# Performance work log

Hardware: AMD Instinct MI355X
Metric: run time of the kernel (lower is better)

Reference implementation:

```python
import jax, jax.numpy as jnp
import numpy as np

N_NODES = 100000
N_EDGES = 300000
HID = 256
N0, N1, N2 = 40000, 30000, 30000
D0, D1, D2 = 512, 256, 128


def setup_inputs() -> dict:
    key = jax.random.key(0)
    ks = jax.random.split(key, 14)
    s = 0.05  # init scale
    return {
        "feat0": jax.random.normal(ks[0], (N0, D0), jnp.float32),
        "feat1": jax.random.normal(ks[1], (N1, D1), jnp.float32),
        "feat2": jax.random.normal(ks[2], (N2, D2), jnp.float32),
        # per-type Linear(in_dim, HID) params (torch Linear: y = x @ W.T + b)
        "fc_w0": jax.random.normal(ks[3], (HID, D0), jnp.float32) * s,
        "fc_b0": jnp.zeros((HID,), jnp.float32),
        "fc_w1": jax.random.normal(ks[4], (HID, D1), jnp.float32) * s,
        "fc_b1": jnp.zeros((HID,), jnp.float32),
        "fc_w2": jax.random.normal(ks[5], (HID, D2), jnp.float32) * s,
        "fc_b2": jnp.zeros((HID,), jnp.float32),
        # GraphConv 1: weight=False, bias=True
        "gc1_bias": jnp.zeros((HID,), jnp.float32),
        # GraphConv 2: weight (in,out) + bias (DGL convention: feat @ W)
        "gc2_weight": jax.random.normal(ks[6], (HID, HID), jnp.float32) * s,
        "gc2_bias": jnp.zeros((HID,), jnp.float32),
        "semantic_weight": jax.random.normal(ks[7], (1, 5), jnp.float32),
        "src": jax.random.randint(ks[8], (N_EDGES,), 0, N_NODES, jnp.int64),
        "dst": jax.random.randint(ks[9], (N_EDGES,), 0, N_NODES, jnp.int64),
    }


def reference(feat0, feat1, feat2, fc_w0, fc_b0, fc_w1, fc_b1, fc_w2, fc_b2,
              gc1_bias, gc2_weight, gc2_bias, semantic_weight, src, dst):
    # per-type projection then concat along node dim -> [N_NODES, HID]
    h = jnp.concatenate([
        feat0 @ fc_w0.T + fc_b0,
        feat1 @ fc_w1.T + fc_b1,
        feat2 @ fc_w2.T + fc_b2,
    ], axis=0)

    ones = jnp.ones((src.shape[0],), h.dtype)
    deg_out = jnp.maximum(jax.ops.segment_sum(ones, src, num_segments=N_NODES), 1.0)
    deg_in = jnp.maximum(jax.ops.segment_sum(ones, dst, num_segments=N_NODES), 1.0)
    norm_out = jax.lax.rsqrt(deg_out)[:, None]  # D_out^{-1/2}
    norm_in = jax.lax.rsqrt(deg_in)[:, None]    # D_in^{-1/2}

    def gconv(x, W, b):
        # DGL GraphConv, norm='both': D_in^{-1/2} A D_out^{-1/2} x W + b, relu
        msg = (x * norm_out)[src]                                  # [E, HID]
        agg = jax.ops.segment_sum(msg, dst, num_segments=N_NODES)  # [N, HID]
        agg = agg * norm_in
        if W is not None:
            agg = agg @ W
        return jax.nn.relu(agg + b)

    # dropout is identity in eval mode
    h = gconv(h, None, gc1_bias)        # layer 0: weight=False
    h = gconv(h, gc2_weight, gc2_bias)  # layer 1
    return h, semantic_weight
```

## Files before the change

### kernel.cpp

```cpp
#include <hip/hip_runtime.h>
#include <cstdint>

#define HID 256
static constexpr int    NNODES = 100000;
static constexpr int    NEDGES = 300000;
static constexpr size_t NH     = (size_t)NNODES * HID;
static constexpr int    SCAN_B = 256;
static constexpr int    NSBLK  = (NNODES + SCAN_B - 1) / SCAN_B;

typedef __attribute__((ext_vector_type(8))) short bf16x8;
typedef __attribute__((ext_vector_type(4))) float f32x4;

__device__ __forceinline__ unsigned short f2bf(float x) {
    unsigned int u = __float_as_uint(x);
    u += 0x7fffu + ((u >> 16) & 1u);
    return (unsigned short)(u >> 16);
}
__device__ __forceinline__ unsigned int pack2(float a, float b) {
    return (unsigned int)f2bf(a) | ((unsigned int)f2bf(b) << 16);
}
__device__ __forceinline__ float bflo(unsigned int u) { return __uint_as_float(u << 16); }
__device__ __forceinline__ float bfhi(unsigned int u) { return __uint_as_float(u & 0xffff0000u); }

__global__ void zero_i32_k(int* __restrict__ p, int n) {
    int i = blockIdx.x * blockDim.x + threadIdx.x;
    if (i < n) p[i] = 0;
}

__global__ void count_deg_k(const int* __restrict__ src, const int* __restrict__ dst,
                            int* __restrict__ degout, int* __restrict__ degin) {
    int e = blockIdx.x * blockDim.x + threadIdx.x;
    if (e < NEDGES) {
        atomicAdd(degout + src[e], 1);
        atomicAdd(degin  + dst[e], 1);
    }
}

__global__ void cvt_weights_k(const float* __restrict__ w0, const float* __restrict__ w1,
                              const float* __restrict__ w2, const float* __restrict__ wg,
                              unsigned short* __restrict__ o0, unsigned short* __restrict__ o1,
                              unsigned short* __restrict__ o2, unsigned short* __restrict__ ogT) {
    int b = blockIdx.x, t = threadIdx.x;
    const float* in; unsigned short* out; int i;
    if (b < 128)      { in = w0; out = o0; i = b * 256 + t; }
    else if (b < 192) { in = w1; out = o1; i = (b - 128) * 256 + t; }
    else if (b < 224) { in = w2; out = o2; i = (b - 192) * 256 + t; }
    else {
        int n = b - 224, k = t;
        ogT[n * 256 + k] = f2bf(wg[k * 256 + n]);
        return;
    }
    float4 v = ((const float4*)in)[i];
    ushort4 w;
    w.x = f2bf(v.x); w.y = f2bf(v.y); w.z = f2bf(v.z); w.w = f2bf(v.w);
    ((ushort4*)out)[i] = w;
}

__global__ void scan_a_k(const int* __restrict__ degin, const int* __restrict__ degout,
                         int* __restrict__ row_off, int* __restrict__ bsums,
                         float* __restrict__ nout, float* __restrict__ nin,
                         const float* __restrict__ sw, float* __restrict__ tail) {
    __shared__ int sm[SCAN_B];
    int t = threadIdx.x;
    int g = blockIdx.x * SCAN_B + t;
    int v = (g < NNODES) ? degin[g] : 0;
    sm[t] = v;
    if (g < NNODES) {
        nout[g] = rsqrtf(fmaxf((float)degout[g], 1.0f));
        nin[g]  = rsqrtf(fmaxf((float)v, 1.0f));
    }
    if (g < 5) tail[g] = sw[g];
    __syncthreads();
#pragma unroll
    for (int off = 1; off < SCAN_B; off <<= 1) {
        int x = (t >= off) ? sm[t - off] : 0;
        __syncthreads();
        sm[t] += x;
        __syncthreads();
    }
    if (g < NNODES) row_off[g] = sm[t] - v;
    if (t == SCAN_B - 1) bsums[blockIdx.x] = sm[t];
}

__global__ void scan_b_k(int* __restrict__ bsums) {
    __shared__ int sm[512];
    int t = threadIdx.x;
    int v = (t < NSBLK) ? bsums[t] : 0;
    sm[t] = v;
    __syncthreads();
#pragma unroll
    for (int off = 1; off < 512; off <<= 1) {
        int x = (t >= off) ? sm[t - off] : 0;
        __syncthreads();
        sm[t] += x;
        __syncthreads();
    }
    if (t < NSBLK) bsums[t] = sm[t] - v;
}

__global__ void scan_c_k(int* __restrict__ row_off, const int* __restrict__ bsums) {
    int g = blockIdx.x * SCAN_B + threadIdx.x;
    if (g < NNODES) row_off[g] += bsums[blockIdx.x];
    if (g == 0) row_off[NNODES] = NEDGES;
}

__global__ void fill_csr_k(const int* __restrict__ src, const int* __restrict__ dst,
                           const int* __restrict__ row_off, int* __restrict__ cursor,
                           int* __restrict__ csr_src) {
    int e = blockIdx.x * blockDim.x + threadIdx.x;
    if (e < NEDGES) {
        int d = dst[e];
        int pos = row_off[d] + atomicAdd(cursor + d, 1);
        csr_src[pos] = src[e];
    }
}

template <int EPI>
__global__ __launch_bounds__(256) void gather_k(
    const unsigned short* __restrict__ h, const int* __restrict__ row_off,
    const int* __restrict__ csr_src, const float* __restrict__ nin,
    const float* __restrict__ bias, void* __restrict__ outv)
{
    int node = blockIdx.x * 4 + (threadIdx.x >> 6);
    if (node >= NNODES) return;
    int lane = threadIdx.x & 63;
    int beg = row_off[node], end = row_off[node + 1];
    float a0 = 0.f, a1 = 0.f, a2 = 0.f, a3 = 0.f;
    const size_t loff = (size_t)lane * 4;
    for (int base = beg; base < end; base += 64) {
        int cnt = end - base; if (cnt > 64) cnt = 64;
        int idx = csr_src[base + (lane < cnt ? lane : cnt - 1)];
        for (int j = 0; j < cnt; j += 8) {
            uint2 v0 = {0,0}, v1 = {0,0}, v2 = {0,0}, v3 = {0,0};
            uint2 v4 = {0,0}, v5 = {0,0}, v6 = {0,0}, v7 = {0,0};
#define GLD(U, VU)                                                              \
            if (j + U < cnt) {                                                  \
                int s = __shfl(idx, j + U);                                     \
                VU = *(const uint2*)(h + (size_t)s * HID + loff);               \
            }
            GLD(0, v0) GLD(1, v1) GLD(2, v2) GLD(3, v3)
            GLD(4, v4) GLD(5, v5) GLD(6, v6) GLD(7, v7)
#undef GLD
            a0 += (bflo(v0.x) + bflo(v1.x)) + (bflo(v2.x) + bflo(v3.x))
                + (bflo(v4.x) + bflo(v5.x)) + (bflo(v6.x) + bflo(v7.x));
            a1 += (bfhi(v0.x) + bfhi(v1.x)) + (bfhi(v2.x) + bfhi(v3.x))
                + (bfhi(v4.x) + bfhi(v5.x)) + (bfhi(v6.x) + bfhi(v7.x));
            a2 += (bflo(v0.y) + bflo(v1.y)) + (bflo(v2.y) + bflo(v3.y))
                + (bflo(v4.y) + bflo(v5.y)) + (bflo(v6.y) + bflo(v7.y));
            a3 += (bfhi(v0.y) + bfhi(v1.y)) + (bfhi(v2.y) + bfhi(v3.y))
                + (bfhi(v4.y) + bfhi(v5.y)) + (bfhi(v6.y) + bfhi(v7.y));
        }
    }
    if (EPI) {
        float ni = nin[node];
        float4 bb = *(const float4*)(bias + lane * 4);
        float4 o;
        o.x = fmaxf(fmaf(a0, ni, bb.x), 0.f);
        o.y = fmaxf(fmaf(a1, ni, bb.y), 0.f);
        o.z = fmaxf(fmaf(a2, ni, bb.z), 0.f);
        o.w = fmaxf(fmaf(a3, ni, bb.w), 0.f);
        *(float4*)((float*)outv + (size_t)node * HID + lane * 4) = o;
    } else {
        ushort4 o;
        o.x = f2bf(a0); o.y = f2bf(a1); o.z = f2bf(a2); o.w = f2bf(a3);
        *(ushort4*)((unsigned short*)outv + (size_t)node * HID + lane * 4) = o;
    }
}

__global__ __launch_bounds__(256, 3) void proj_mfma_k(
    const float* __restrict__ f0, const float* __restrict__ f1, const float* __restrict__ f2,
    const unsigned short* __restrict__ w0, const unsigned short* __restrict__ w1,
    const unsigned short* __restrict__ w2,
    const float* __restrict__ b0, const float* __restrict__ b1, const float* __restrict__ b2,
    const float* __restrict__ nout, unsigned short* __restrict__ h0)
{
    __shared__ unsigned short As[2][64 * 32];

    int bx = blockIdx.x;
    const float* A; const unsigned short* B; const float* bias; const float* rs;
    unsigned short* C; int M, K;
    if (bx < 625)       { A = f0; B = w0; bias = b0; rs = nout;          C = h0;                          M = 40000; K = 512; }
    else if (bx < 1094) { bx -= 625;  A = f1; B = w1; bias = b1; rs = nout + 40000; C = h0 + (size_t)40000 * HID; M = 30000; K = 256; }
    else                { bx -= 1094; A = f2; B = w2; bias = b2; rs = nout + 70000; C = h0 + (size_t)70000 * HID; M = 30000; K = 128; }
    const int m0 = bx * 64;

    const int tid  = threadIdx.x;
    const int wn   = tid >> 6;
    const int lane = tid & 63;
    const int half = lane >> 4;
    const int l15  = lane & 15;

    f32x4 acc[4][4];
#pragma unroll
    for (int i = 0; i < 4; ++i)
#pragma unroll
        for (int j = 0; j < 4; ++j)
#pragma unroll
            for (int r = 0; r < 4; ++r) acc[i][j][r] = 0.f;

    const int arow = tid >> 2, ac = tid & 3;
    const int aslot = ac ^ ((arow >> 1) & 3);
    int agm = m0 + arow; if (agm > M - 1) agm = M - 1;
    const float* ap = A + (size_t)agm * K + ac * 8;

    const unsigned short* bp = B + (size_t)(wn * 64 + l15 * 4) * K + half * 8;

    const int nT = K >> 5;

    float4 a0 = *(const float4*)ap;
    float4 a1 = *(const float4*)(ap + 4);
    bf16x8 bcur[4];
#pragma unroll
    for (int j = 0; j < 4; ++j) bcur[j] = *(const bf16x8*)(bp + (size_t)j * K);

    for (int t = 0; t < nT; ++t) {
        const int p = t & 1;
        {
            uint4 u;
            u.x = pack2(a0.x, a0.y); u.y = pack2(a0.z, a0.w);
            u.z = pack2(a1.x, a1.y); u.w = pack2(a1.z, a1.w);
            *(uint4*)&As[p][(arow * 4 + aslot) * 8] = u;
        }
        asm volatile("s_waitcnt lgkmcnt(0)" ::: "memory");
        __builtin_amdgcn_s_barrier();
        asm volatile("" ::: "memory");
        __builtin_amdgcn_sched_barrier(0);

        const int tn = (t + 1 < nT) ? t + 1 : t;
        {
            const float* pn = ap + tn * 32;
            a0 = *(const float4*)pn;
            a1 = *(const float4*)(pn + 4);
        }
        bf16x8 bnext[4];
#pragma unroll
        for (int j = 0; j < 4; ++j)
            bnext[j] = *(const bf16x8*)(bp + (size_t)j * K + tn * 32);

        bf16x8 af[4];
#pragma unroll
        for (int i = 0; i < 4; ++i) {
            int m = i * 16 + l15;
            int ca = half ^ ((m >> 1) & 3);
            af[i] = *(const bf16x8*)&As[p][(m * 4 + ca) * 8];
        }
#pragma unroll
        for (int i = 0; i < 4; ++i)
#pragma unroll
            for (int j = 0; j < 4; ++j)
                acc[i][j] = __builtin_amdgcn_mfma_f32_16x16x32_bf16(
                    af[i], bcur[j], acc[i][j], 0, 0, 0);
#pragma unroll
        for (int j = 0; j < 4; ++j) bcur[j] = bnext[j];
    }

    float4 bb = *(const float4*)(bias + wn * 64 + l15 * 4);
#pragma unroll
    for (int i = 0; i < 4; ++i) {
        int mb = m0 + i * 16 + half * 4;
        if (mb >= M) continue;
        float4 rv = *(const float4*)(rs + mb);
#pragma unroll
        for (int r = 0; r < 4; ++r) {
            float rsm = (&rv.x)[r];
            ushort4 o;
            o.x = f2bf((acc[i][0][r] + bb.x) * rsm);
            o.y = f2bf((acc[i][1][r] + bb.y) * rsm);
            o.z = f2bf((acc[i][2][r] + bb.z) * rsm);
            o.w = f2bf((acc[i][3][r] + bb.w) * rsm);
            *(ushort4*)&C[(size_t)(mb + r) * HID + wn * 64 + l15 * 4] = o;
        }
    }
}

__global__ __launch_bounds__(256, 3) void mid_mfma_k(
    const unsigned short* __restrict__ agg1, const unsigned short* __restrict__ wT,
    const float* __restrict__ b1, const float* __restrict__ nin,
    const float* __restrict__ nout, unsigned short* __restrict__ h2)
{
    __shared__ unsigned short As[2][64 * 32];

    const int m0   = blockIdx.x * 64;
    const int tid  = threadIdx.x;
    const int wn   = tid >> 6;
    const int lane = tid & 63;
    const int half = lane >> 4;
    const int l15  = lane & 15;

    f32x4 acc[4][4];
#pragma unroll
    for (int i = 0; i < 4; ++i)
#pragma unroll
        for (int j = 0; j < 4; ++j)
#pragma unroll
            for (int r = 0; r < 4; ++r) acc[i][j][r] = 0.f;

    const int arow = tid >> 2, ac = tid & 3;
    const int aslot = ac ^ ((arow >> 1) & 3);
    int agm = m0 + arow; if (agm > NNODES - 1) agm = NNODES - 1;
    const float ni = nin[agm], no = nout[agm];
    const unsigned short* ap = agg1 + (size_t)agm * HID + ac * 8;
    const unsigned short* bp = wT + (size_t)(wn * 64 + l15 * 4) * 256 + half * 8;

    uint4 au = *(const uint4*)ap;
    bf16x8 bcur[4];
#pragma unroll
    for (int j = 0; j < 4; ++j) bcur[j] = *(const bf16x8*)(bp + j * 256);

#pragma unroll 2
    for (int t = 0; t < 8; ++t) {
        const int p = t & 1;
        {
            const int k0 = t * 32;
            float4 c0 = *(const float4*)(b1 + k0 + ac * 8);
            float4 c1 = *(const float4*)(b1 + k0 + ac * 8 + 4);
            float x0 = fmaxf(fmaf(bflo(au.x), ni, c0.x), 0.f) * no;
            float x1 = fmaxf(fmaf(bfhi(au.x), ni, c0.y), 0.f) * no;
            float x2 = fmaxf(fmaf(bflo(au.y), ni, c0.z), 0.f) * no;
            float x3 = fmaxf(fmaf(bfhi(au.y), ni, c0.w), 0.f) * no;
            float x4 = fmaxf(fmaf(bflo(au.z), ni, c1.x), 0.f) * no;
            float x5 = fmaxf(fmaf(bfhi(au.z), ni, c1.y), 0.f) * no;
            float x6 = fmaxf(fmaf(bflo(au.w), ni, c1.z), 0.f) * no;
            float x7 = fmaxf(fmaf(bfhi(au.w), ni, c1.w), 0.f) * no;
            uint4 o;
            o.x = pack2(x0, x1); o.y = pack2(x2, x3);
            o.z = pack2(x4, x5); o.w = pack2(x6, x7);
            *(uint4*)&As[p][(arow * 4 + aslot) * 8] = o;
        }
        asm volatile("s_waitcnt lgkmcnt(0)" ::: "memory");
        __builtin_amdgcn_s_barrier();
        asm volatile("" ::: "memory");
        __builtin_amdgcn_sched_barrier(0);

        const int tn = (t + 1 < 8) ? t + 1 : t;
        au = *(const uint4*)(ap + tn * 32);
        bf16x8 bnext[4];
#pragma unroll
        for (int j = 0; j < 4; ++j)
            bnext[j] = *(const bf16x8*)(bp + j * 256 + tn * 32);

        bf16x8 af[4];
#pragma unroll
        for (int i = 0; i < 4; ++i) {
            int m = i * 16 + l15;
            int ca = half ^ ((m >> 1) & 3);
            af[i] = *(const bf16x8*)&As[p][(m * 4 + ca) * 8];
        }
#pragma unroll
        for (int i = 0; i < 4; ++i)
#pragma unroll
            for (int j = 0; j < 4; ++j)
                acc[i][j] = __builtin_amdgcn_mfma_f32_16x16x32_bf16(
                    af[i], bcur[j], acc[i][j], 0, 0, 0);
#pragma unroll
        for (int j = 0; j < 4; ++j) bcur[j] = bnext[j];
    }

#pragma unroll
    for (int i = 0; i < 4; ++i) {
        int mb = m0 + i * 16 + half * 4;
        if (mb >= NNODES) continue;
#pragma unroll
        for (int r = 0; r < 4; ++r) {
            ushort4 o;
            o.x = f2bf(acc[i][0][r]);
            o.y = f2bf(acc[i][1][r]);
            o.z = f2bf(acc[i][2][r]);
            o.w = f2bf(acc[i][3][r]);
            *(ushort4*)&h2[(size_t)(mb + r) * HID + wn * 64 + l15 * 4] = o;
        }
    }
}

extern "C" void kernel_launch(void* const* d_in, const int* in_sizes, int n_in,
                              void* d_out, int out_size, void* d_ws, size_t ws_size,
                              hipStream_t stream)
{
    const float* feat0    = (const float*)d_in[0];
    const float* feat1    = (const float*)d_in[1];
    const float* feat2    = (const float*)d_in[2];
    const float* fc_w0    = (const float*)d_in[3];
    const float* fc_b0    = (const float*)d_in[4];
    const float* fc_w1    = (const float*)d_in[5];
    const float* fc_b1    = (const float*)d_in[6];
    const float* fc_w2    = (const float*)d_in[7];
    const float* fc_b2    = (const float*)d_in[8];
    const float* gc1_bias = (const float*)d_in[9];
    const float* gc2_w    = (const float*)d_in[10];
    const float* gc2_bias = (const float*)d_in[11];
    const float* sw       = (const float*)d_in[12];
    const int*   src      = (const int*)d_in[13];
    const int*   dst      = (const int*)d_in[14];

    unsigned short* h0b  = (unsigned short*)d_ws;
    unsigned short* agg1 = h0b + NH;
    unsigned short* h2b  = h0b;
    unsigned short* w0b  = agg1 + NH;
    unsigned short* w1b  = w0b + 131072;
    unsigned short* w2b  = w1b + 65536;
    unsigned short* w2Tb = w2b + 32768;
    float* nout = (float*)(w2Tb + 65536);
    float* nin  = nout + NNODES;
    int* deg_out = (int*)(nin + NNODES);
    int* deg_in  = deg_out + NNODES;
    int* cursor  = deg_in + NNODES;
    int* row_off = cursor + NNODES;
    int* bsums   = row_off + NNODES + 1;
    int* csr_src = bsums + 512;
    float* out   = (float*)d_out;

    zero_i32_k<<<(3 * NNODES + 255) / 256, 256, 0, stream>>>(deg_out, 3 * NNODES);
    cvt_weights_k<<<480, 256, 0, stream>>>(fc_w0, fc_w1, fc_w2, gc2_w,
                                           w0b, w1b, w2b, w2Tb);
    count_deg_k<<<(NEDGES + 255) / 256, 256, 0, stream>>>(src, dst, deg_out, deg_in);
    scan_a_k<<<NSBLK, SCAN_B, 0, stream>>>(deg_in, deg_out, row_off, bsums,
                                           nout, nin, sw, out + NH);
    scan_b_k<<<1, 512, 0, stream>>>(bsums);
    scan_c_k<<<NSBLK, SCAN_B, 0, stream>>>(row_off, bsums);
    fill_csr_k<<<(NEDGES + 255) / 256, 256, 0, stream>>>(src, dst, row_off, cursor, csr_src);

    proj_mfma_k<<<1563, 256, 0, stream>>>(feat0, feat1, feat2, w0b, w1b, w2b,
                                          fc_b0, fc_b1, fc_b2, nout, h0b);

    gather_k<0><<<(NNODES + 3) / 4, 256, 0, stream>>>(h0b, row_off, csr_src,
                                                      nullptr, nullptr, agg1);

    mid_mfma_k<<<1563, 256, 0, stream>>>(agg1, w2Tb, gc1_bias, nin, nout, h2b);

    gather_k<1><<<(NNODES + 3) / 4, 256, 0, stream>>>(h2b, row_off, csr_src,
                                                      nin, gc2_bias, out);
}
```

Baseline: 396.9 us.

## Split-K projection tiles for type-0 features and persistent grid-stride gather

The feat0 projection (K=512) now uses 32-row tiles where two wave pairs each cover half of K and half of N, and the partial sums are combined through shared memory. This doubles the block count for that segment to improve load balance and shorten each block's serial K loop. The gather kernels become persistent, grid-stride loops over 2048 blocks that prefetch the next node's CSR row offsets and load the bias once. The cost is extra LDS traffic and barriers for the split-K reduction, and B fragments are no longer software-prefetched in the new path.

```diff
diff --git a/kernel.cpp b/kernel.cpp
--- a/kernel.cpp
+++ b/kernel.cpp
@@ -121,49 +121,61 @@
     const int* __restrict__ csr_src, const float* __restrict__ nin,
     const float* __restrict__ bias, void* __restrict__ outv)
 {
-    int node = blockIdx.x * 4 + (threadIdx.x >> 6);
-    if (node >= NNODES) return;
-    int lane = threadIdx.x & 63;
-    int beg = row_off[node], end = row_off[node + 1];
-    float a0 = 0.f, a1 = 0.f, a2 = 0.f, a3 = 0.f;
+    const int nslots = gridDim.x * 4;
+    const int wslot  = blockIdx.x * 4 + (threadIdx.x >> 6);
+    const int lane   = threadIdx.x & 63;
     const size_t loff = (size_t)lane * 4;
-    for (int base = beg; base < end; base += 64) {
-        int cnt = end - base; if (cnt > 64) cnt = 64;
-        int idx = csr_src[base + (lane < cnt ? lane : cnt - 1)];
-        for (int j = 0; j < cnt; j += 8) {
-            uint2 v0 = {0,0}, v1 = {0,0}, v2 = {0,0}, v3 = {0,0};
-            uint2 v4 = {0,0}, v5 = {0,0}, v6 = {0,0}, v7 = {0,0};
+    float4 bb;
+    if (EPI) bb = *(const float4*)(bias + lane * 4);
+
+    int node = wslot;
+    int beg = 0, end = 0;
+    if (node < NNODES) { beg = row_off[node]; end = row_off[node + 1]; }
+
+    while (node < NNODES) {
+        const int nnode = node + nslots;
+        int nbeg = 0, nend = 0;
+        if (nnode < NNODES) { nbeg = row_off[nnode]; nend = row_off[nnode + 1]; }
+
+        float a0 = 0.f, a1 = 0.f, a2 = 0.f, a3 = 0.f;
+        for (int base = beg; base < end; base += 64) {
+            int cnt = end - base; if (cnt > 64) cnt = 64;
+            int idx = csr_src[base + (lane < cnt ? lane : cnt - 1)];
+            for (int j = 0; j < cnt; j += 8) {
+                uint2 v0 = {0,0}, v1 = {0,0}, v2 = {0,0}, v3 = {0,0};
+                uint2 v4 = {0,0}, v5 = {0,0}, v6 = {0,0}, v7 = {0,0};
 #define GLD(U, VU)                                                              \
-            if (j + U < cnt) {                                                  \
-                int s = __shfl(idx, j + U);                                     \
-                VU = *(const uint2*)(h + (size_t)s * HID + loff);               \
-            }
-            GLD(0, v0) GLD(1, v1) GLD(2, v2) GLD(3, v3)
-            GLD(4, v4) GLD(5, v5) GLD(6, v6) GLD(7, v7)
+                if (j + U < cnt) {                                              \
+                    int s = __shfl(idx, j + U);                                 \
+                    VU = *(const uint2*)(h + (size_t)s * HID + loff);           \
+                }
+                GLD(0, v0) GLD(1, v1) GLD(2, v2) GLD(3, v3)
+                GLD(4, v4) GLD(5, v5) GLD(6, v6) GLD(7, v7)
 #undef GLD
-            a0 += (bflo(v0.x) + bflo(v1.x)) + (bflo(v2.x) + bflo(v3.x))
-                + (bflo(v4.x) + bflo(v5.x)) + (bflo(v6.x) + bflo(v7.x));
-            a1 += (bfhi(v0.x) + bfhi(v1.x)) + (bfhi(v2.x) + bfhi(v3.x))
-                + (bfhi(v4.x) + bfhi(v5.x)) + (bfhi(v6.x) + bfhi(v7.x));
-            a2 += (bflo(v0.y) + bflo(v1.y)) + (bflo(v2.y) + bflo(v3.y))
-                + (bflo(v4.y) + bflo(v5.y)) + (bflo(v6.y) + bflo(v7.y));
-            a3 += (bfhi(v0.y) + bfhi(v1.y)) + (bfhi(v2.y) + bfhi(v3.y))
-                + (bfhi(v4.y) + bfhi(v5.y)) + (bfhi(v6.y) + bfhi(v7.y));
-        }
-    }
-    if (EPI) {
-        float ni = nin[node];
-        float4 bb = *(const float4*)(bias + lane * 4);
-        float4 o;
-        o.x = fmaxf(fmaf(a0, ni, bb.x), 0.f);
-        o.y = fmaxf(fmaf(a1, ni, bb.y), 0.f);
-        o.z = fmaxf(fmaf(a2, ni, bb.z), 0.f);
-        o.w = fmaxf(fmaf(a3, ni, bb.w), 0.f);
-        *(float4*)((float*)outv + (size_t)node * HID + lane * 4) = o;
-    } else {
-        ushort4 o;
-        o.x = f2bf(a0); o.y = f2bf(a1); o.z = f2bf(a2); o.w = f2bf(a3);
-        *(ushort4*)((unsigned short*)outv + (size_t)node * HID + lane * 4) = o;
+                a0 += (bflo(v0.x) + bflo(v1.x)) + (bflo(v2.x) + bflo(v3.x))
+                    + (bflo(v4.x) + bflo(v5.x)) + (bflo(v6.x) + bflo(v7.x));
+                a1 += (bfhi(v0.x) + bfhi(v1.x)) + (bfhi(v2.x) + bfhi(v3.x))
+                    + (bfhi(v4.x) + bfhi(v5.x)) + (bfhi(v6.x) + bfhi(v7.x));
+                a2 += (bflo(v0.y) + bflo(v1.y)) + (bflo(v2.y) + bflo(v3.y))
+                    + (bflo(v4.y) + bflo(v5.y)) + (bflo(v6.y) + bflo(v7.y));
+                a3 += (bfhi(v0.y) + bfhi(v1.y)) + (bfhi(v2.y) + bfhi(v3.y))
+                    + (bfhi(v4.y) + bfhi(v5.y)) + (bfhi(v6.y) + bfhi(v7.y));
+            }
+        }
+        if (EPI) {
+            float ni = nin[node];
+            float4 o;
+            o.x = fmaxf(fmaf(a0, ni, bb.x), 0.f);
+            o.y = fmaxf(fmaf(a1, ni, bb.y), 0.f);
+            o.z = fmaxf(fmaf(a2, ni, bb.z), 0.f);
+            o.w = fmaxf(fmaf(a3, ni, bb.w), 0.f);
+            *(float4*)((float*)outv + (size_t)node * HID + lane * 4) = o;
+        } else {
+            ushort4 o;
+            o.x = f2bf(a0); o.y = f2bf(a1); o.z = f2bf(a2); o.w = f2bf(a3);
+            *(ushort4*)((unsigned short*)outv + (size_t)node * HID + lane * 4) = o;
+        }
+        node = nnode; beg = nbeg; end = nend;
     }
 }
 
@@ -174,21 +186,133 @@
     const float* __restrict__ b0, const float* __restrict__ b1, const float* __restrict__ b2,
     const float* __restrict__ nout, unsigned short* __restrict__ h0)
 {
-    __shared__ unsigned short As[2][64 * 32];
+    __shared__ unsigned short smem[12288];
 
     int bx = blockIdx.x;
-    const float* A; const unsigned short* B; const float* bias; const float* rs;
-    unsigned short* C; int M, K;
-    if (bx < 625)       { A = f0; B = w0; bias = b0; rs = nout;          C = h0;                          M = 40000; K = 512; }
-    else if (bx < 1094) { bx -= 625;  A = f1; B = w1; bias = b1; rs = nout + 40000; C = h0 + (size_t)40000 * HID; M = 30000; K = 256; }
-    else                { bx -= 1094; A = f2; B = w2; bias = b2; rs = nout + 70000; C = h0 + (size_t)70000 * HID; M = 30000; K = 128; }
-    const int m0 = bx * 64;
-
     const int tid  = threadIdx.x;
-    const int wn   = tid >> 6;
+    const int wid  = tid >> 6;
     const int lane = tid & 63;
     const int half = lane >> 4;
     const int l15  = lane & 15;
+
+    if (bx < 1250) {
+        const int m0    = bx * 32;
+        const int khalf = wid >> 1;
+        const int nhf   = wid & 1;
+
+        f32x4 acc[2][8];
+#pragma unroll
+        for (int i = 0; i < 2; ++i)
+#pragma unroll
+            for (int j = 0; j < 8; ++j)
+#pragma unroll
+                for (int r = 0; r < 4; ++r) acc[i][j][r] = 0.f;
+
+        const int pan  = tid >> 7;
+        const int q    = tid & 127;
+        const int arow = q >> 2;
+        const int ac   = q & 3;
+        const int aslot = ac ^ ((arow >> 1) & 3);
+        const float* ap = f0 + (size_t)(m0 + arow) * 512 + pan * 256 + ac * 8;
+
+        const unsigned short* bp = w0 + (size_t)(nhf * 128 + l15 * 4) * 512 + khalf * 256 + half * 8;
+
+        float4 a0v = *(const float4*)ap;
+        float4 a1v = *(const float4*)(ap + 4);
+
+        for (int t = 0; t < 8; ++t) {
+            const int p = t & 1;
+            {
+                uint4 u;
+                u.x = pack2(a0v.x, a0v.y); u.y = pack2(a0v.z, a0v.w);
+                u.z = pack2(a1v.x, a1v.y); u.w = pack2(a1v.z, a1v.w);
+                *(uint4*)&smem[(p * 2 + pan) * 1024 + (arow * 4 + aslot) * 8] = u;
+            }
+            asm volatile("s_waitcnt lgkmcnt(0)" ::: "memory");
+            __builtin_amdgcn_s_barrier();
+            asm volatile("" ::: "memory");
+            __builtin_amdgcn_sched_barrier(0);
+
+            const int tn = (t + 1 < 8) ? t + 1 : t;
+            {
+                const float* pn = ap + tn * 32;
+                a0v = *(const float4*)pn;
+                a1v = *(const float4*)(pn + 4);
+            }
+            bf16x8 bfr[8];
+#pragma unroll
+            for (int jj = 0; jj < 8; ++jj)
+                bfr[jj] = *(const bf16x8*)(bp + (size_t)((jj >> 2) * 64 + (jj & 3)) * 512 + t * 32);
+
+            bf16x8 af[2];
+#pragma unroll
+            for (int i = 0; i < 2; ++i) {
+                int m = i * 16 + l15;
+                int ca = half ^ ((m >> 1) & 3);
+                af[i] = *(const bf16x8*)&smem[(p * 2 + khalf) * 1024 + (m * 4 + ca) * 8];
+            }
+#pragma unroll
+            for (int i = 0; i < 2; ++i)
+#pragma unroll
+                for (int jj = 0; jj < 8; ++jj)
+                    acc[i][jj] = __builtin_amdgcn_mfma_f32_16x16x32_bf16(
+                        af[i], bfr[jj], acc[i][jj], 0, 0, 0);
+        }
+
+        f32x4* cmb = (f32x4*)&smem[4096];
+#pragma unroll
+        for (int rnd = 0; rnd < 2; ++rnd) {
+            __syncthreads();
+            if (khalf == 1) {
+#pragma unroll
+                for (int j = 0; j < 8; ++j)
+                    cmb[(nhf * 64 + lane) * 8 + j] = acc[rnd][j];
+            }
+            __syncthreads();
+            if (khalf == 0) {
+#pragma unroll
+                for (int j = 0; j < 8; ++j) {
+                    f32x4 v = cmb[(nhf * 64 + lane) * 8 + j];
+#pragma unroll
+                    for (int r = 0; r < 4; ++r) acc[rnd][j][r] += v[r];
+                }
+            }
+        }
+
+        if (khalf == 0) {
+            float4 bq0 = *(const float4*)(b0 + nhf * 128 + l15 * 4);
+            float4 bq1 = *(const float4*)(b0 + nhf * 128 + 64 + l15 * 4);
+#pragma unroll
+            for (int i = 0; i < 2; ++i) {
+                int mb = m0 + i * 16 + half * 4;
+                float4 rv = *(const float4*)(nout + mb);
+#pragma unroll
+                for (int r = 0; r < 4; ++r) {
+                    float rsm = (&rv.x)[r];
+                    ushort4 o;
+                    o.x = f2bf((acc[i][0][r] + bq0.x) * rsm);
+                    o.y = f2bf((acc[i][1][r] + bq0.y) * rsm);
+                    o.z = f2bf((acc[i][2][r] + bq0.z) * rsm);
+                    o.w = f2bf((acc[i][3][r] + bq0.w) * rsm);
+                    *(ushort4*)&h0[(size_t)(mb + r) * HID + nhf * 128 + l15 * 4] = o;
+                    ushort4 o2;
+                    o2.x = f2bf((acc[i][4][r] + bq1.x) * rsm);
+                    o2.y = f2bf((acc[i][5][r] + bq1.y) * rsm);
+                    o2.z = f2bf((acc[i][6][r] + bq1.z) * rsm);
+                    o2.w = f2bf((acc[i][7][r] + bq1.w) * rsm);
+                    *(ushort4*)&h0[(size_t)(mb + r) * HID + nhf * 128 + 64 + l15 * 4] = o2;
+                }
+            }
+        }
+        return;
+    }
+
+    const float* A; const unsigned short* B; const float* bias; const float* rs;
+    unsigned short* C; int M, K;
+    if (bx < 1719) { bx -= 1250; A = f1; B = w1; bias = b1; rs = nout + 40000; C = h0 + (size_t)40000 * HID; M = 30000; K = 256; }
+    else           { bx -= 1719; A = f2; B = w2; bias = b2; rs = nout + 70000; C = h0 + (size_t)70000 * HID; M = 30000; K = 128; }
+    const int m0 = bx * 64;
+    const int wn = wid;
 
     f32x4 acc[4][4];
 #pragma unroll
@@ -219,7 +343,7 @@
             uint4 u;
             u.x = pack2(a0.x, a0.y); u.y = pack2(a0.z, a0.w);
             u.z = pack2(a1.x, a1.y); u.w = pack2(a1.z, a1.w);
-            *(uint4*)&As[p][(arow * 4 + aslot) * 8] = u;
+            *(uint4*)&smem[p * 2048 + (arow * 4 + aslot) * 8] = u;
         }
         asm volatile("s_waitcnt lgkmcnt(0)" ::: "memory");
         __builtin_amdgcn_s_barrier();
@@ -242,7 +366,7 @@
         for (int i = 0; i < 4; ++i) {
             int m = i * 16 + l15;
             int ca = half ^ ((m >> 1) & 3);
-            af[i] = *(const bf16x8*)&As[p][(m * 4 + ca) * 8];
+            af[i] = *(const bf16x8*)&smem[p * 2048 + (m * 4 + ca) * 8];
         }
 #pragma unroll
         for (int i = 0; i < 4; ++i)
@@ -419,14 +543,14 @@
     scan_c_k<<<NSBLK, SCAN_B, 0, stream>>>(row_off, bsums);
     fill_csr_k<<<(NEDGES + 255) / 256, 256, 0, stream>>>(src, dst, row_off, cursor, csr_src);
 
-    proj_mfma_k<<<1563, 256, 0, stream>>>(feat0, feat1, feat2, w0b, w1b, w2b,
+    proj_mfma_k<<<2188, 256, 0, stream>>>(feat0, feat1, feat2, w0b, w1b, w2b,
                                           fc_b0, fc_b1, fc_b2, nout, h0b);
 
-    gather_k<0><<<(NNODES + 3) / 4, 256, 0, stream>>>(h0b, row_off, csr_src,
-                                                      nullptr, nullptr, agg1);
+    gather_k<0><<<2048, 256, 0, stream>>>(h0b, row_off, csr_src,
+                                          nullptr, nullptr, agg1);
 
     mid_mfma_k<<<1563, 256, 0, stream>>>(agg1, w2Tb, gc1_bias, nin, nout, h2b);
 
-    gather_k<1><<<(NNODES + 3) / 4, 256, 0, stream>>>(h2b, row_off, csr_src,
-                                                      nin, gc2_bias, out);
-}
+    gather_k<1><<<2048, 256, 0, stream>>>(h2b, row_off, csr_src,
+                                          nin, gc2_bias, out);
+}
```

Result: slower. 414.8 us (+4.5%).

## Load MFMA A-fragments straight from global and make gather persistent

Applied to the files above, without the earlier changes.

The projection and middle GEMM kernels drop the LDS staging buffer, the barriers and the double-buffered prefetch. Each lane now loads its own A-fragment rows from global memory, converts them to bf16 and feeds the MFMA directly. The gather kernels become grid-stride persistent loops over 2048 blocks, prefetching the next node's CSR row offsets and loading the bias once. This removes LDS traffic and barrier stalls, but A rows are now fetched redundantly by all four waves and there is no explicit software prefetch of A and B.

```diff
diff --git a/kernel.cpp b/kernel.cpp
--- a/kernel.cpp
+++ b/kernel.cpp
@@ -121,49 +121,61 @@
     const int* __restrict__ csr_src, const float* __restrict__ nin,
     const float* __restrict__ bias, void* __restrict__ outv)
 {
-    int node = blockIdx.x * 4 + (threadIdx.x >> 6);
-    if (node >= NNODES) return;
-    int lane = threadIdx.x & 63;
-    int beg = row_off[node], end = row_off[node + 1];
-    float a0 = 0.f, a1 = 0.f, a2 = 0.f, a3 = 0.f;
+    const int nslots = gridDim.x * 4;
+    const int wslot  = blockIdx.x * 4 + (threadIdx.x >> 6);
+    const int lane   = threadIdx.x & 63;
     const size_t loff = (size_t)lane * 4;
-    for (int base = beg; base < end; base += 64) {
-        int cnt = end - base; if (cnt > 64) cnt = 64;
-        int idx = csr_src[base + (lane < cnt ? lane : cnt - 1)];
-        for (int j = 0; j < cnt; j += 8) {
-            uint2 v0 = {0,0}, v1 = {0,0}, v2 = {0,0}, v3 = {0,0};
-            uint2 v4 = {0,0}, v5 = {0,0}, v6 = {0,0}, v7 = {0,0};
+    float4 bb;
+    if (EPI) bb = *(const float4*)(bias + lane * 4);
+
+    int node = wslot;
+    int beg = 0, end = 0;
+    if (node < NNODES) { beg = row_off[node]; end = row_off[node + 1]; }
+
+    while (node < NNODES) {
+        const int nnode = node + nslots;
+        int nbeg = 0, nend = 0;
+        if (nnode < NNODES) { nbeg = row_off[nnode]; nend = row_off[nnode + 1]; }
+
+        float a0 = 0.f, a1 = 0.f, a2 = 0.f, a3 = 0.f;
+        for (int base = beg; base < end; base += 64) {
+            int cnt = end - base; if (cnt > 64) cnt = 64;
+            int idx = csr_src[base + (lane < cnt ? lane : cnt - 1)];
+            for (int j = 0; j < cnt; j += 8) {
+                uint2 v0 = {0,0}, v1 = {0,0}, v2 = {0,0}, v3 = {0,0};
+                uint2 v4 = {0,0}, v5 = {0,0}, v6 = {0,0}, v7 = {0,0};
 #define GLD(U, VU)                                                              \
-            if (j + U < cnt) {                                                  \
-                int s = __shfl(idx, j + U);                                     \
-                VU = *(const uint2*)(h + (size_t)s * HID + loff);               \
+                if (j + U < cnt) {                                              \
+                    int s = __shfl(idx, j + U);                                 \
+                    VU = *(const uint2*)(h + (size_t)s * HID + loff);           \
+                }
+                GLD(0, v0) GLD(1, v1) GLD(2, v2) GLD(3, v3)
+                GLD(4, v4) GLD(5, v5) GLD(6, v6) GLD(7, v7)
+#undef GLD
+                a0 += (bflo(v0.x) + bflo(v1.x)) + (bflo(v2.x) + bflo(v3.x))
+                    + (bflo(v4.x) + bflo(v5.x)) + (bflo(v6.x) + bflo(v7.x));
+                a1 += (bfhi(v0.x) + bfhi(v1.x)) + (bfhi(v2.x) + bfhi(v3.x))
+                    + (bfhi(v4.x) + bfhi(v5.x)) + (bfhi(v6.x) + bfhi(v7.x));
+                a2 += (bflo(v0.y) + bflo(v1.y)) + (bflo(v2.y) + bflo(v3.y))
+                    + (bflo(v4.y) + bflo(v5.y)) + (bflo(v6.y) + bflo(v7.y));
+                a3 += (bfhi(v0.y) + bfhi(v1.y)) + (bfhi(v2.y) + bfhi(v3.y))
+                    + (bfhi(v4.y) + bfhi(v5.y)) + (bfhi(v6.y) + bfhi(v7.y));
             }
-            GLD(0, v0) GLD(1, v1) GLD(2, v2) GLD(3, v3)
-            GLD(4, v4) GLD(5, v5) GLD(6, v6) GLD(7, v7)
-#undef GLD
-            a0 += (bflo(v0.x) + bflo(v1.x)) + (bflo(v2.x) + bflo(v3.x))
-                + (bflo(v4.x) + bflo(v5.x)) + (bflo(v6.x) + bflo(v7.x));
-            a1 += (bfhi(v0.x) + bfhi(v1.x)) + (bfhi(v2.x) + bfhi(v3.x))
-                + (bfhi(v4.x) + bfhi(v5.x)) + (bfhi(v6.x) + bfhi(v7.x));
-            a2 += (bflo(v0.y) + bflo(v1.y)) + (bflo(v2.y) + bflo(v3.y))
-                + (bflo(v4.y) + bflo(v5.y)) + (bflo(v6.y) + bflo(v7.y));
-            a3 += (bfhi(v0.y) + bfhi(v1.y)) + (bfhi(v2.y) + bfhi(v3.y))
-                + (bfhi(v4.y) + bfhi(v5.y)) + (bfhi(v6.y) + bfhi(v7.y));
-        }
-    }
-    if (EPI) {
-        float ni = nin[node];
-        float4 bb = *(const float4*)(bias + lane * 4);
-        float4 o;
-        o.x = fmaxf(fmaf(a0, ni, bb.x), 0.f);
-        o.y = fmaxf(fmaf(a1, ni, bb.y), 0.f);
-        o.z = fmaxf(fmaf(a2, ni, bb.z), 0.f);
-        o.w = fmaxf(fmaf(a3, ni, bb.w), 0.f);
-        *(float4*)((float*)outv + (size_t)node * HID + lane * 4) = o;
-    } else {
-        ushort4 o;
-        o.x = f2bf(a0); o.y = f2bf(a1); o.z = f2bf(a2); o.w = f2bf(a3);
-        *(ushort4*)((unsigned short*)outv + (size_t)node * HID + lane * 4) = o;
+        }
+        if (EPI) {
+            float ni = nin[node];
+            float4 o;
+            o.x = fmaxf(fmaf(a0, ni, bb.x), 0.f);
+            o.y = fmaxf(fmaf(a1, ni, bb.y), 0.f);
+            o.z = fmaxf(fmaf(a2, ni, bb.z), 0.f);
+            o.w = fmaxf(fmaf(a3, ni, bb.w), 0.f);
+            *(float4*)((float*)outv + (size_t)node * HID + lane * 4) = o;
+        } else {
+            ushort4 o;
+            o.x = f2bf(a0); o.y = f2bf(a1); o.z = f2bf(a2); o.w = f2bf(a3);
+            *(ushort4*)((unsigned short*)outv + (size_t)node * HID + lane * 4) = o;
+        }
+        node = nnode; beg = nbeg; end = nend;
     }
 }
 
@@ -174,8 +186,6 @@
     const float* __restrict__ b0, const float* __restrict__ b1, const float* __restrict__ b2,
     const float* __restrict__ nout, unsigned short* __restrict__ h0)
 {
-    __shared__ unsigned short As[2][64 * 32];
-
     int bx = blockIdx.x;
     const float* A; const unsigned short* B; const float* bias; const float* rs;
     unsigned short* C; int M, K;
@@ -198,60 +208,36 @@
 #pragma unroll
             for (int r = 0; r < 4; ++r) acc[i][j][r] = 0.f;
 
-    const int arow = tid >> 2, ac = tid & 3;
-    const int aslot = ac ^ ((arow >> 1) & 3);
-    int agm = m0 + arow; if (agm > M - 1) agm = M - 1;
-    const float* ap = A + (size_t)agm * K + ac * 8;
-
+    const float* arp[4];
+#pragma unroll
+    for (int i = 0; i < 4; ++i) {
+        int m = m0 + i * 16 + l15; if (m > M - 1) m = M - 1;
+        arp[i] = A + (size_t)m * K + half * 8;
+    }
     const unsigned short* bp = B + (size_t)(wn * 64 + l15 * 4) * K + half * 8;
 
     const int nT = K >> 5;
-
-    float4 a0 = *(const float4*)ap;
-    float4 a1 = *(const float4*)(ap + 4);
-    bf16x8 bcur[4];
-#pragma unroll
-    for (int j = 0; j < 4; ++j) bcur[j] = *(const bf16x8*)(bp + (size_t)j * K);
-
+#pragma unroll 2
     for (int t = 0; t < nT; ++t) {
-        const int p = t & 1;
-        {
-            uint4 u;
-            u.x = pack2(a0.x, a0.y); u.y = pack2(a0.z, a0.w);
-            u.z = pack2(a1.x, a1.y); u.w = pack2(a1.z, a1.w);
-            *(uint4*)&As[p][(arow * 4 + aslot) * 8] = u;
-        }
-        asm volatile("s_waitcnt lgkmcnt(0)" ::: "memory");
-        __builtin_amdgcn_s_barrier();
-        asm volatile("" ::: "memory");
-        __builtin_amdgcn_sched_barrier(0);
-
-        const int tn = (t + 1 < nT) ? t + 1 : t;
-        {
-            const float* pn = ap + tn * 32;
-            a0 = *(const float4*)pn;
-            a1 = *(const float4*)(pn + 4);
-        }
-        bf16x8 bnext[4];
+        bf16x8 bfv[4];
 #pragma unroll
         for (int j = 0; j < 4; ++j)
-            bnext[j] = *(const bf16x8*)(bp + (size_t)j * K + tn * 32);
-
-        bf16x8 af[4];
+            bfv[j] = *(const bf16x8*)(bp + (size_t)j * K + t * 32);
 #pragma unroll
         for (int i = 0; i < 4; ++i) {
-            int m = i * 16 + l15;
-            int ca = half ^ ((m >> 1) & 3);
-            af[i] = *(const bf16x8*)&As[p][(m * 4 + ca) * 8];
-        }
-#pragma unroll
-        for (int i = 0; i < 4; ++i)
+            const float* p = arp[i] + t * 32;
+            float4 v0 = *(const float4*)p;
+            float4 v1 = *(const float4*)(p + 4);
+            union { unsigned int u[4]; bf16x8 v; } af;
+            af.u[0] = pack2(v0.x, v0.y);
+            af.u[1] = pack2(v0.z, v0.w);
+            af.u[2] = pack2(v1.x, v1.y);
+            af.u[3] = pack2(v1.z, v1.w);
 #pragma unroll
             for (int j = 0; j < 4; ++j)
                 acc[i][j] = __builtin_amdgcn_mfma_f32_16x16x32_bf16(
-                    af[i], bcur[j], acc[i][j], 0, 0, 0);
-#pragma unroll
-        for (int j = 0; j < 4; ++j) bcur[j] = bnext[j];
+                    af.v, bfv[j], acc[i][j], 0, 0, 0);
+        }
     }
 
     float4 bb = *(const float4*)(bias + wn * 64 + l15 * 4);
@@ -278,8 +264,6 @@
     const float* __restrict__ b1, const float* __restrict__ nin,
     const float* __restrict__ nout, unsigned short* __restrict__ h2)
 {
-    __shared__ unsigned short As[2][64 * 32];
-
     const int m0   = blockIdx.x * 64;
     const int tid  = threadIdx.x;
     const int wn   = tid >> 6;
@@ -295,65 +279,45 @@
 #pragma unroll
             for (int r = 0; r < 4; ++r) acc[i][j][r] = 0.f;
 
-    const int arow = tid >> 2, ac = tid & 3;
-    const int aslot = ac ^ ((arow >> 1) & 3);
-    int agm = m0 + arow; if (agm > NNODES - 1) agm = NNODES - 1;
-    const float ni = nin[agm], no = nout[agm];
-    const unsigned short* ap = agg1 + (size_t)agm * HID + ac * 8;
+    const unsigned short* arp[4];
+    float ni[4], no[4];
+#pragma unroll
+    for (int i = 0; i < 4; ++i) {
+        int m = m0 + i * 16 + l15; if (m > NNODES - 1) m = NNODES - 1;
+        arp[i] = agg1 + (size_t)m * HID + half * 8;
+        ni[i] = nin[m]; no[i] = nout[m];
+    }
     const unsigned short* bp = wT + (size_t)(wn * 64 + l15 * 4) * 256 + half * 8;
-
-    uint4 au = *(const uint4*)ap;
-    bf16x8 bcur[4];
-#pragma unroll
-    for (int j = 0; j < 4; ++j) bcur[j] = *(const bf16x8*)(bp + j * 256);
 
 #pragma unroll 2
     for (int t = 0; t < 8; ++t) {
-        const int p = t & 1;
-        {
-            const int k0 = t * 32;
-            float4 c0 = *(const float4*)(b1 + k0 + ac * 8);
-            float4 c1 = *(const float4*)(b1 + k0 + ac * 8 + 4);
-            float x0 = fmaxf(fmaf(bflo(au.x), ni, c0.x), 0.f) * no;
-            float x1 = fmaxf(fmaf(bfhi(au.x), ni, c0.y), 0.f) * no;
-            float x2 = fmaxf(fmaf(bflo(au.y), ni, c0.z), 0.f) * no;
-            float x3 = fmaxf(fmaf(bfhi(au.y), ni, c0.w), 0.f) * no;
-            float x4 = fmaxf(fmaf(bflo(au.z), ni, c1.x), 0.f) * no;
-            float x5 = fmaxf(fmaf(bfhi(au.z), ni, c1.y), 0.f) * no;
-            float x6 = fmaxf(fmaf(bflo(au.w), ni, c1.z), 0.f) * no;
-            float x7 = fmaxf(fmaf(bfhi(au.w), ni, c1.w), 0.f) * no;
-            uint4 o;
-            o.x = pack2(x0, x1); o.y = pack2(x2, x3);
-            o.z = pack2(x4, x5); o.w = pack2(x6, x7);
-            *(uint4*)&As[p][(arow * 4 + aslot) * 8] = o;
-        }
-        asm volatile("s_waitcnt lgkmcnt(0)" ::: "memory");
-        __builtin_amdgcn_s_barrier();
-        asm volatile("" ::: "memory");
-        __builtin_amdgcn_sched_barrier(0);
-
-        const int tn = (t + 1 < 8) ? t + 1 : t;
-        au = *(const uint4*)(ap + tn * 32);
-        bf16x8 bnext[4];
+        bf16x8 bfv[4];
 #pragma unroll
         for (int j = 0; j < 4; ++j)
-            bnext[j] = *(const bf16x8*)(bp + j * 256 + tn * 32);
-
-        bf16x8 af[4];
+            bfv[j] = *(const bf16x8*)(bp + j * 256 + t * 32);
+        float4 c0 = *(const float4*)(b1 + t * 32 + half * 8);
+        float4 c1 = *(const float4*)(b1 + t * 32 + half * 8 + 4);
 #pragma unroll
         for (int i = 0; i < 4; ++i) {
-            int m = i * 16 + l15;
-            int ca = half ^ ((m >> 1) & 3);
-            af[i] = *(const bf16x8*)&As[p][(m * 4 + ca) * 8];
-        }
-#pragma unroll
-        for (int i = 0; i < 4; ++i)
+            uint4 u = *(const uint4*)(arp[i] + t * 32);
+            float x0 = fmaxf(fmaf(bflo(u.x), ni[i], c0.x), 0.f) * no[i];
+            float x1 = fmaxf(fmaf(bfhi(u.x), ni[i], c0.y), 0.f) * no[i];
+            float x2 = fmaxf(fmaf(bflo(u.y), ni[i], c0.z), 0.f) * no[i];
+            float x3 = fmaxf(fmaf(bfhi(u.y), ni[i], c0.w), 0.f) * no[i];
+            float x4 = fmaxf(fmaf(bflo(u.z), ni[i], c1.x), 0.f) * no[i];
+            float x5 = fmaxf(fmaf(bfhi(u.z), ni[i], c1.y), 0.f) * no[i];
+            float x6 = fmaxf(fmaf(bflo(u.w), ni[i], c1.z), 0.f) * no[i];
+            float x7 = fmaxf(fmaf(bfhi(u.w), ni[i], c1.w), 0.f) * no[i];
+            union { unsigned int u[4]; bf16x8 v; } af;
+            af.u[0] = pack2(x0, x1);
+            af.u[1] = pack2(x2, x3);
+            af.u[2] = pack2(x4, x5);
+            af.u[3] = pack2(x6, x7);
 #pragma unroll
             for (int j = 0; j < 4; ++j)
                 acc[i][j] = __builtin_amdgcn_mfma_f32_16x16x32_bf16(
-                    af[i], bcur[j], acc[i][j], 0, 0, 0);
-#pragma unroll
-        for (int j = 0; j < 4; ++j) bcur[j] = bnext[j];
+                    af.v, bfv[j], acc[i][j], 0, 0, 0);
+        }
     }
 
 #pragma unroll
@@ -422,11 +386,11 @@
     proj_mfma_k<<<1563, 256, 0, stream>>>(feat0, feat1, feat2, w0b, w1b, w2b,
                                           fc_b0, fc_b1, fc_b2, nout, h0b);
 
-    gather_k<0><<<(NNODES + 3) / 4, 256, 0, stream>>>(h0b, row_off, csr_src,
-                                                      nullptr, nullptr, agg1);
+    gather_k<0><<<2048, 256, 0, stream>>>(h0b, row_off, csr_src,
+                                          nullptr, nullptr, agg1);
 
     mid_mfma_k<<<1563, 256, 0, stream>>>(agg1, w2Tb, gc1_bias, nin, nout, h2b);
 
-    gather_k<1><<<(NNODES + 3) / 4, 256, 0, stream>>>(h2b, row_off, csr_src,
-                                                      nin, gc2_bias, out);
-}
+    gather_k<1><<<2048, 256, 0, stream>>>(h2b, row_off, csr_src,
+                                          nin, gc2_bias, out);
+}
```

Result: slower. 462.7 us (+16.6%).
